# Kernel tuning notes

Measured on AMD Instinct MI355X. Metric: run time of the kernel, lower is better.

The kernel has to match this reference:

```python
import jax, jax.numpy as jnp
import numpy as np

B, S, D_IN, D_OUT, E = 4, 2048, 1024, 1024, 8

def setup_inputs() -> dict:
    key = jax.random.key(0)
    ks = jax.random.split(key, 5)
    scale = 1.0 / np.sqrt(D_IN)
    x  = jax.random.normal(ks[0], (B, S, D_IN), dtype=jnp.float32)
    We = jax.random.uniform(ks[1], (E, D_OUT, D_IN), dtype=jnp.float32, minval=-scale, maxval=scale)
    be = jax.random.uniform(ks[2], (E, D_OUT), dtype=jnp.float32, minval=-scale, maxval=scale)
    Wg = jax.random.uniform(ks[3], (E, D_IN), dtype=jnp.float32, minval=-scale, maxval=scale)
    bg = jax.random.uniform(ks[4], (E,), dtype=jnp.float32, minval=-scale, maxval=scale)
    return {"x": x, "We": We, "be": be, "Wg": Wg, "bg": bg}

def reference(x, We, be, Wg, bg):
    # gate: [B,S,E]
    gate_logits = jnp.einsum('bsd,ed->bse', x, Wg) + bg
    gate = jax.nn.softmax(gate_logits, axis=-1)
    top1 = jnp.argmax(gate, axis=-1)                      # [B,S]
    one_hot = jax.nn.one_hot(top1, E, dtype=x.dtype)      # [B,S,E]
    # all-expert dense outputs, stacked on last axis: [B,S,O,E]
    expert_outs = jnp.einsum('bsd,eod->bsoe', x, We) + be.T
    out = jnp.einsum('bsoe,bse->bso', expert_outs, one_hot)
    mean_gate = gate.mean(axis=(0, 1))                    # [E]
    aux_loss = jnp.mean((mean_gate * E) ** 2)
    return (out, aux_loss)
```

## Files before the change

kernel.cpp:

```cpp
#include <hip/hip_runtime.h>
#include <hip/hip_bf16.h>


#define NTOK 8192
#define DIN  1024
#define DOUT 1024
#define NE   8

typedef unsigned short u16;
typedef unsigned int   u32;
typedef unsigned long long u64;
typedef short  bf16x8 __attribute__((ext_vector_type(8)));
typedef float  f32x4  __attribute__((ext_vector_type(4)));

__device__ __forceinline__ u16 f2bf(float f) {
    __hip_bfloat16 h = __float2bfloat16(f);
    return *(u16*)&h;
}


__global__ __launch_bounds__(256) void gate_kernel(
    const float* __restrict__ x, const float* __restrict__ Wg,
    const float* __restrict__ bg, u32* __restrict__ stage)
{
    __shared__ int   am_s[16];
    __shared__ float mg_s[4][NE];

    const int tid  = threadIdx.x;
    const int wave = tid >> 6;
    const int lane = tid & 63;
    const int g    = lane >> 3;
    const int sub  = lane & 7;

    const float* wr = Wg + g * DIN + 4 * sub;

    float bgl[NE];
    #pragma unroll
    for (int e = 0; e < NE; ++e) bgl[e] = bg[e];

    float mgacc = 0.f;

    #pragma unroll 1
    for (int it = 0; it < 4; ++it) {
        const int t = blockIdx.x * 16 + wave * 4 + it;
        const float* xr = x + (size_t)t * DIN + 4 * sub;

        float acc0 = 0.f, acc1 = 0.f, acc2 = 0.f, acc3 = 0.f;
        #pragma unroll
        for (int j = 0; j < 8; ++j) {
            const int k = j * 128;
            f32x4 x0 = *(const f32x4*)(xr + k);
            f32x4 w0 = *(const f32x4*)(wr + k);
            f32x4 x1 = *(const f32x4*)(xr + k + 32);
            f32x4 w1 = *(const f32x4*)(wr + k + 32);
            f32x4 x2 = *(const f32x4*)(xr + k + 64);
            f32x4 w2 = *(const f32x4*)(wr + k + 64);
            f32x4 x3 = *(const f32x4*)(xr + k + 96);
            f32x4 w3 = *(const f32x4*)(wr + k + 96);
            #pragma unroll
            for (int q = 0; q < 4; ++q) {
                acc0 = fmaf(w0[q], x0[q], acc0);
                acc1 = fmaf(w1[q], x1[q], acc1);
                acc2 = fmaf(w2[q], x2[q], acc2);
                acc3 = fmaf(w3[q], x3[q], acc3);
            }
        }
        float acc = (acc0 + acc1) + (acc2 + acc3);

        acc += __shfl_xor(acc, 1, 64);
        acc += __shfl_xor(acc, 2, 64);
        acc += __shfl_xor(acc, 4, 64);

        float logit[NE];
        #pragma unroll
        for (int e = 0; e < NE; ++e)
            logit[e] = __shfl(acc, e * 8, 64) + bgl[e];

        float m = logit[0]; int am = 0;
        #pragma unroll
        for (int e = 1; e < NE; ++e) if (logit[e] > m) { m = logit[e]; am = e; }

        float p[NE], s = 0.f;
        #pragma unroll
        for (int e = 0; e < NE; ++e) { p[e] = __expf(logit[e] - m); s += p[e]; }
        const float inv = 1.f / s;

        float psel = p[0];
        #pragma unroll
        for (int e = 1; e < NE; ++e) psel = (lane == e) ? p[e] : psel;
        if (lane < NE) mgacc += psel * inv;

        if (lane == 0) am_s[wave * 4 + it] = am;
    }

    if (lane < NE) mg_s[wave][lane] = mgacc;
    __syncthreads();

    u32* rec = stage + (size_t)blockIdx.x * 16;
    if (tid == 0) {
        u64 pack = 0;
        #pragma unroll
        for (int i = 0; i < 16; ++i) pack |= (u64)am_s[i] << (4 * i);
        *(u64*)rec = pack;
    }
    if (tid < NE) {
        float s = mg_s[0][tid] + mg_s[1][tid] + mg_s[2][tid] + mg_s[3][tid];
        rec[2 + tid] = __float_as_uint(s);
    }
}

__global__ __launch_bounds__(512) void route_kernel(
    const u32* __restrict__ stage, int* __restrict__ counts,
    int* __restrict__ tok_list, float* __restrict__ out)
{
    __shared__ float mgl[512][NE];
    __shared__ int   c[512][9];
    __shared__ float tot_s[NE];

    const int tid  = threadIdx.x;
    const int wave = tid >> 6;
    const int lane = tid & 63;

    const u64 pack = *(const u64*)(stage + (size_t)tid * 16);
    #pragma unroll
    for (int e = 0; e < NE; ++e)
        mgl[tid][e] = __uint_as_float(stage[tid * 16 + 2 + e]);

    #pragma unroll
    for (int e = 0; e < 9; ++e) c[tid][e] = 0;

    #pragma unroll
    for (int it = 0; it < 16; ++it) {
        int e3 = (int)((pack >> (4 * it)) & 7);
        c[tid][e3]++;
    }
    __syncthreads();

    {
        const int e = wave;
        int carry = 0;
        #pragma unroll 1
        for (int ch = 0; ch < 8; ++ch) {
            int v = c[ch * 64 + lane][e];
            int incl = v;
            #pragma unroll
            for (int off = 1; off < 64; off <<= 1) {
                int n = __shfl_up(incl, off, 64);
                if (lane >= off) incl += n;
            }
            c[ch * 64 + lane][e] = incl - v + carry;
            carry += __shfl(incl, 63, 64);
        }
        if (lane == 0) counts[e] = carry;
    }
    __syncthreads();

    #pragma unroll
    for (int it = 0; it < 16; ++it) {
        int e3 = (int)((pack >> (4 * it)) & 7);
        int pos = c[tid][e3]++;
        tok_list[e3 * NTOK + pos] = tid * 16 + it;
    }

    {
        const int e = wave;
        float s = 0.f;
        #pragma unroll
        for (int ch = 0; ch < 8; ++ch) s += mgl[ch * 64 + lane][e];
        #pragma unroll
        for (int off = 32; off > 0; off >>= 1) s += __shfl_xor(s, off, 64);
        if (lane == 0) tot_s[e] = s;
    }
    __syncthreads();
    if (tid == 0) {
        float s = 0.f;
        #pragma unroll
        for (int e = 0; e < NE; ++e) {
            float m = tot_s[e] * (8.0f / 8192.0f);
            s += m * m;
        }
        out[(size_t)NTOK * DOUT] = s * 0.125f;
    }
}

__global__ __launch_bounds__(256) void moe_gemm(
    const float* __restrict__ x, const float* __restrict__ We,
    const float* __restrict__ be, const int* __restrict__ counts,
    const int* __restrict__ tok_list, float* __restrict__ out)
{
    const int e   = blockIdx.z;
    const int cnt = counts[e];
    const int m0  = blockIdx.y * 128;
    if (m0 >= cnt) return;
    const int n0  = blockIdx.x * 128;

    __shared__ u16 sA[128 * 32];
    __shared__ u16 sB[128 * 32];
    __shared__ int toks[128];

    const int tid = threadIdx.x;
    if (tid < 128) {
        int gr = m0 + tid;
        toks[tid] = (gr < cnt) ? tok_list[e * NTOK + gr] : tok_list[e * NTOK];
    }
    __syncthreads();

    const int lane = tid & 63;
    const int wave = tid >> 6;
    const int wm   = (wave & 1) * 64;
    const int wn   = (wave >> 1) * 64;
    const int lrow = lane & 15;
    const int quad = lane >> 4;

    f32x4 acc[4][4];
    #pragma unroll
    for (int i = 0; i < 4; ++i)
        #pragma unroll
        for (int j = 0; j < 4; ++j) acc[i][j] = (f32x4){0.f, 0.f, 0.f, 0.f};

    const int srow  = tid >> 1;
    const int shalf = (tid & 1) * 16;

    const float* xrow = x  + (size_t)toks[srow] * DIN + shalf;
    const float* brow = We + ((size_t)e << 20) + ((size_t)(n0 + srow) << 10) + shalf;

    #pragma unroll 1
    for (int k0 = 0; k0 < DIN; k0 += 32) {
        f32x4 a[4], b[4];
        #pragma unroll
        for (int q = 0; q < 4; ++q) {
            a[q] = *(const f32x4*)(xrow + k0 + 4 * q);
            b[q] = *(const f32x4*)(brow + k0 + 4 * q);
        }
        union { u16 h[16]; uint4 u[2]; } pa, pb;
        #pragma unroll
        for (int q = 0; q < 4; ++q)
            #pragma unroll
            for (int j = 0; j < 4; ++j) {
                pa.h[q * 4 + j] = f2bf(a[q][j]);
                pb.h[q * 4 + j] = f2bf(b[q][j]);
            }
        *(uint4*)&sA[srow * 32 + shalf]     = pa.u[0];
        *(uint4*)&sA[srow * 32 + shalf + 8] = pa.u[1];
        *(uint4*)&sB[srow * 32 + shalf]     = pb.u[0];
        *(uint4*)&sB[srow * 32 + shalf + 8] = pb.u[1];
        __syncthreads();

        bf16x8 af[4], bfr[4];
        #pragma unroll
        for (int i = 0; i < 4; ++i)
            af[i] = *(const bf16x8*)&sA[(wm + i * 16 + lrow) * 32 + quad * 8];
        #pragma unroll
        for (int j = 0; j < 4; ++j)
            bfr[j] = *(const bf16x8*)&sB[(wn + j * 16 + lrow) * 32 + quad * 8];
        #pragma unroll
        for (int i = 0; i < 4; ++i)
            #pragma unroll
            for (int j = 0; j < 4; ++j)
                acc[i][j] = __builtin_amdgcn_mfma_f32_16x16x32_bf16(
                    af[i], bfr[j], acc[i][j], 0, 0, 0);
        __syncthreads();
    }

    #pragma unroll
    for (int j = 0; j < 4; ++j) {
        const int col = n0 + wn + j * 16 + lrow;
        const float bev = be[e * DOUT + col];
        #pragma unroll
        for (int i = 0; i < 4; ++i) {
            #pragma unroll
            for (int r = 0; r < 4; ++r) {
                const int rl = wm + i * 16 + quad * 4 + r;
                if (m0 + rl < cnt) {
                    const int tok = toks[rl];
                    out[((size_t)tok << 10) + col] = acc[i][j][r] + bev;
                }
            }
        }
    }
}

extern "C" void kernel_launch(void* const* d_in, const int* in_sizes, int n_in,
                              void* d_out, int out_size, void* d_ws, size_t ws_size,
                              hipStream_t stream) {
    const float* x  = (const float*)d_in[0];
    const float* We = (const float*)d_in[1];
    const float* be = (const float*)d_in[2];
    const float* Wg = (const float*)d_in[3];
    const float* bg = (const float*)d_in[4];
    float* out = (float*)d_out;

    int* counts   = (int*)d_ws;
    int* tok_list = (int*)((char*)d_ws + 256);
    u32* stage    = (u32*)((char*)d_ws + 256);

    gate_kernel<<<512, 256, 0, stream>>>(x, Wg, bg, stage);
    route_kernel<<<1, 512, 0, stream>>>(stage, counts, tok_list, out);
    moe_gemm<<<dim3(8, 64, 8), 256, 0, stream>>>(x, We, be, counts, tok_list, out);
}
```

Before: 187.0 us.

## Retile MoE GEMM to 64x128 with K=64, XOR-swizzled LDS and register prefetch

Measured after the change: 182.0 us. 1.03x faster.

```diff
diff --git a/kernel.cpp b/kernel.cpp
--- a/kernel.cpp
+++ b/kernel.cpp
@@ -190,16 +190,16 @@
 {
     const int e   = blockIdx.z;
     const int cnt = counts[e];
-    const int m0  = blockIdx.y * 128;
+    const int m0  = blockIdx.y * 64;
     if (m0 >= cnt) return;
     const int n0  = blockIdx.x * 128;
 
-    __shared__ u16 sA[128 * 32];
-    __shared__ u16 sB[128 * 32];
-    __shared__ int toks[128];
+    __shared__ u16 sA[64 * 64];
+    __shared__ u16 sB[128 * 64];
+    __shared__ int toks[64];
 
     const int tid = threadIdx.x;
-    if (tid < 128) {
+    if (tid < 64) {
         int gr = m0 + tid;
         toks[tid] = (gr < cnt) ? tok_list[e * NTOK + gr] : tok_list[e * NTOK];
     }
@@ -207,70 +207,116 @@
 
     const int lane = tid & 63;
     const int wave = tid >> 6;
-    const int wm   = (wave & 1) * 64;
-    const int wn   = (wave >> 1) * 64;
+    const int wn   = wave * 32;
     const int lrow = lane & 15;
     const int quad = lane >> 4;
-
-    f32x4 acc[4][4];
+    const int l7   = lrow & 7;
+
+    f32x4 acc[4][2];
     #pragma unroll
     for (int i = 0; i < 4; ++i)
         #pragma unroll
-        for (int j = 0; j < 4; ++j) acc[i][j] = (f32x4){0.f, 0.f, 0.f, 0.f};
-
-    const int srow  = tid >> 1;
-    const int shalf = (tid & 1) * 16;
-
-    const float* xrow = x  + (size_t)toks[srow] * DIN + shalf;
-    const float* brow = We + ((size_t)e << 20) + ((size_t)(n0 + srow) << 10) + shalf;
-
+        for (int j = 0; j < 2; ++j) acc[i][j] = (f32x4){0.f, 0.f, 0.f, 0.f};
+
+    const int srow = tid >> 3;
+    const int ch   = tid & 7;
+    const int cx   = ch ^ (srow & 7);
+
+    const float* aS[2];
+    const float* bS[4];
+    #pragma unroll
+    for (int s = 0; s < 2; ++s)
+        aS[s] = x + (size_t)toks[srow + 32 * s] * DIN + ch * 8;
+    #pragma unroll
+    for (int s = 0; s < 4; ++s)
+        bS[s] = We + ((size_t)e << 20) + ((size_t)(n0 + srow + 32 * s) << 10) + ch * 8;
+
+    f32x4 ar[2][2], br[4][2];
+
+    #define LOADR(k0)                                            \
+        do {                                                     \
+            _Pragma("unroll")                                    \
+            for (int s = 0; s < 2; ++s) {                        \
+                ar[s][0] = *(const f32x4*)(aS[s] + (k0));        \
+                ar[s][1] = *(const f32x4*)(aS[s] + (k0) + 4);    \
+            }                                                    \
+            _Pragma("unroll")                                    \
+            for (int s = 0; s < 4; ++s) {                        \
+                br[s][0] = *(const f32x4*)(bS[s] + (k0));        \
+                br[s][1] = *(const f32x4*)(bS[s] + (k0) + 4);    \
+            }                                                    \
+        } while (0)
+
+    #define STOREW()                                                     \
+        do {                                                             \
+            _Pragma("unroll")                                            \
+            for (int s = 0; s < 2; ++s) {                                \
+                union { u16 h[8]; uint4 u; } ua;                         \
+                _Pragma("unroll")                                        \
+                for (int q = 0; q < 4; ++q) {                            \
+                    ua.h[q]     = f2bf(ar[s][0][q]);                     \
+                    ua.h[4 + q] = f2bf(ar[s][1][q]);                     \
+                }                                                        \
+                *(uint4*)&sA[(srow + 32 * s) * 64 + cx * 8] = ua.u;      \
+            }                                                            \
+            _Pragma("unroll")                                            \
+            for (int s = 0; s < 4; ++s) {                                \
+                union { u16 h[8]; uint4 u; } ub;                         \
+                _Pragma("unroll")                                        \
+                for (int q = 0; q < 4; ++q) {                            \
+                    ub.h[q]     = f2bf(br[s][0][q]);                     \
+                    ub.h[4 + q] = f2bf(br[s][1][q]);                     \
+                }                                                        \
+                *(uint4*)&sB[(srow + 32 * s) * 64 + cx * 8] = ub.u;      \
+            }                                                            \
+        } while (0)
+
+    #define COMPUTE()                                                         \
+        do {                                                                  \
+            bf16x8 af[2][4], bv[2][2];                                        \
+            _Pragma("unroll")                                                 \
+            for (int ks = 0; ks < 2; ++ks) {                                  \
+                const int so = ((ks * 4 + quad) ^ l7) * 8;                    \
+                _Pragma("unroll")                                             \
+                for (int i = 0; i < 4; ++i)                                   \
+                    af[ks][i] = *(const bf16x8*)&sA[(i * 16 + lrow) * 64 + so]; \
+                _Pragma("unroll")                                             \
+                for (int j = 0; j < 2; ++j)                                   \
+                    bv[ks][j] = *(const bf16x8*)&sB[(wn + j * 16 + lrow) * 64 + so]; \
+            }                                                                 \
+            _Pragma("unroll")                                                 \
+            for (int ks = 0; ks < 2; ++ks)                                    \
+                _Pragma("unroll")                                             \
+                for (int i = 0; i < 4; ++i)                                   \
+                    _Pragma("unroll")                                         \
+                    for (int j = 0; j < 2; ++j)                               \
+                        acc[i][j] = __builtin_amdgcn_mfma_f32_16x16x32_bf16(  \
+                            af[ks][i], bv[ks][j], acc[i][j], 0, 0, 0);        \
+        } while (0)
+
+    LOADR(0);
     #pragma unroll 1
-    for (int k0 = 0; k0 < DIN; k0 += 32) {
-        f32x4 a[4], b[4];
-        #pragma unroll
-        for (int q = 0; q < 4; ++q) {
-            a[q] = *(const f32x4*)(xrow + k0 + 4 * q);
-            b[q] = *(const f32x4*)(brow + k0 + 4 * q);
-        }
-        union { u16 h[16]; uint4 u[2]; } pa, pb;
-        #pragma unroll
-        for (int q = 0; q < 4; ++q)
-            #pragma unroll
-            for (int j = 0; j < 4; ++j) {
-                pa.h[q * 4 + j] = f2bf(a[q][j]);
-                pb.h[q * 4 + j] = f2bf(b[q][j]);
-            }
-        *(uint4*)&sA[srow * 32 + shalf]     = pa.u[0];
-        *(uint4*)&sA[srow * 32 + shalf + 8] = pa.u[1];
-        *(uint4*)&sB[srow * 32 + shalf]     = pb.u[0];
-        *(uint4*)&sB[srow * 32 + shalf + 8] = pb.u[1];
+    for (int k0 = 0; k0 < DIN; k0 += 64) {
         __syncthreads();
-
-        bf16x8 af[4], bfr[4];
-        #pragma unroll
-        for (int i = 0; i < 4; ++i)
-            af[i] = *(const bf16x8*)&sA[(wm + i * 16 + lrow) * 32 + quad * 8];
-        #pragma unroll
-        for (int j = 0; j < 4; ++j)
-            bfr[j] = *(const bf16x8*)&sB[(wn + j * 16 + lrow) * 32 + quad * 8];
-        #pragma unroll
-        for (int i = 0; i < 4; ++i)
-            #pragma unroll
-            for (int j = 0; j < 4; ++j)
-                acc[i][j] = __builtin_amdgcn_mfma_f32_16x16x32_bf16(
-                    af[i], bfr[j], acc[i][j], 0, 0, 0);
+        STOREW();
+        if (k0 + 64 < DIN) LOADR(k0 + 64);
         __syncthreads();
-    }
-
-    #pragma unroll
-    for (int j = 0; j < 4; ++j) {
+        COMPUTE();
+    }
+
+    #undef LOADR
+    #undef STOREW
+    #undef COMPUTE
+
+    #pragma unroll
+    for (int j = 0; j < 2; ++j) {
         const int col = n0 + wn + j * 16 + lrow;
         const float bev = be[e * DOUT + col];
         #pragma unroll
         for (int i = 0; i < 4; ++i) {
             #pragma unroll
             for (int r = 0; r < 4; ++r) {
-                const int rl = wm + i * 16 + quad * 4 + r;
+                const int rl = i * 16 + quad * 4 + r;
                 if (m0 + rl < cnt) {
                     const int tok = toks[rl];
                     out[((size_t)tok << 10) + col] = acc[i][j][r] + bev;
@@ -296,5 +342,5 @@
 
     gate_kernel<<<512, 256, 0, stream>>>(x, Wg, bg, stage);
     route_kernel<<<1, 512, 0, stream>>>(stage, counts, tok_list, out);
-    moe_gemm<<<dim3(8, 64, 8), 256, 0, stream>>>(x, We, be, counts, tok_list, out);
-}
+    moe_gemm<<<dim3(8, 128, 8), 256, 0, stream>>>(x, We, be, counts, tok_list, out);
+}
```
